# Kernel optimization log

Hardware: AMD Instinct MI355X
Metric: run time of the kernel (lower is better)

Reference implementation:

```python
import jax, jax.numpy as jnp
import numpy as np
import math

EMB = 768
B, S = 8, 2048

def setup_inputs() -> dict:
    key = jax.random.key(0)
    ks = jax.random.split(key, 6)
    q = jax.random.normal(ks[0], (B, S, EMB), dtype=jnp.float32)
    k = jax.random.normal(ks[1], (B, S, EMB), dtype=jnp.float32)
    v = jax.random.normal(ks[2], (B, S, EMB), dtype=jnp.float32)
    mask = jax.random.randint(ks[3], (B, S, S), 0, 2, dtype=jnp.int32)
    # nn.Linear(emb, emb): weight [out, in], bias [out]
    bound = 1.0 / math.sqrt(EMB)
    W = jax.random.uniform(ks[4], (EMB, EMB), minval=-bound, maxval=bound, dtype=jnp.float32)
    b = jax.random.uniform(ks[5], (EMB,), minval=-bound, maxval=bound, dtype=jnp.float32)
    return {"q": q, "k": k, "v": v, "mask": mask, "W": W, "b": b}

def reference(q, k, v, mask, W, b):
    # shared linear projection (torch Linear: x @ W^T + b)
    qp = jnp.einsum('bse,oe->bso', q, W) + b
    kp = jnp.einsum('bse,oe->bso', k, W) + b
    vp = jnp.einsum('bse,oe->bso', v, W) + b
    scores = jnp.einsum('bqe,bke->bqk', qp, kp) / math.sqrt(EMB)  # [B,S,S]
    scores = jnp.where(mask == 1, -jnp.inf, scores)
    attn = jax.nn.softmax(scores, axis=-1)
    return jnp.einsum('bqk,bke->bqe', attn, vp)
```

## Files before the change

kernel.cpp:

```cpp
#include <hip/hip_runtime.h>
#include <hip/hip_bf16.h>
#include <stdint.h>

#define B_ 8
#define S_ 2048
#define E_ 768

typedef __attribute__((ext_vector_type(4))) float f32x4;
typedef __attribute__((ext_vector_type(8))) short bf16x8;

#define A_TILE_USH (256 * 64)
#define B_TILE_USH (128 * 64)

__device__ __forceinline__ unsigned short f2bf(float f) {
  union { float f; unsigned u; } v; v.f = f;
  unsigned r = v.u + 0x7FFFu + ((v.u >> 16) & 1u);
  return (unsigned short)(r >> 16);
}

__device__ __forceinline__ void gll16(const void* g, void* l) {
  __builtin_amdgcn_global_load_lds((const __attribute__((address_space(1))) void*)g,
                                   (__attribute__((address_space(3))) void*)l, 16, 0, 0);
}

__device__ __forceinline__ void stage_tile(const char* Ab, const char* Bb,
                                           int ldAb, int ldBb, int kt,
                                           unsigned short* As, unsigned short* Bs, int tid) {
#pragma unroll
  for (int i = 0; i < 4; ++i) {
    const unsigned lin = (unsigned)i * 8192u + (unsigned)tid * 16u;
    const unsigned row = lin >> 7, cb = lin & 127u;
    const unsigned cbs = cb ^ ((row & 7u) << 4);
    gll16(Ab + (size_t)row * ldAb + (size_t)kt * 128 + cbs, (char*)As + lin);
  }
#pragma unroll
  for (int i = 0; i < 2; ++i) {
    const unsigned lin = (unsigned)i * 8192u + (unsigned)tid * 16u;
    const unsigned row = lin >> 7, cb = lin & 127u;
    const unsigned cbs = cb ^ ((row & 7u) << 4);
    gll16(Bb + (size_t)row * ldBb + (size_t)kt * 128 + cbs, (char*)Bs + lin);
  }
}

__device__ __forceinline__ void compute_tile(const unsigned short* As, const unsigned short* Bs,
                                             int wm, int wn, int lane, f32x4 (&acc)[4][4]) {
  bf16x8 af[4][2], bv[4][2];
#pragma unroll
  for (int m = 0; m < 4; ++m) {
    const int row = wm * 64 + m * 16 + (lane & 15);
#pragma unroll
    for (int ks = 0; ks < 2; ++ks) {
      const unsigned cb = ((unsigned)ks * 64u + (unsigned)(lane >> 4) * 16u) ^ (((unsigned)row & 7u) << 4);
      af[m][ks] = *reinterpret_cast<const bf16x8*>((const char*)As + row * 128 + cb);
    }
  }
#pragma unroll
  for (int n = 0; n < 4; ++n) {
    const int row = wn * 64 + n * 16 + (lane & 15);
#pragma unroll
    for (int ks = 0; ks < 2; ++ks) {
      const unsigned cb = ((unsigned)ks * 64u + (unsigned)(lane >> 4) * 16u) ^ (((unsigned)row & 7u) << 4);
      bv[n][ks] = *reinterpret_cast<const bf16x8*>((const char*)Bs + row * 128 + cb);
    }
  }
  __builtin_amdgcn_s_setprio(1);
#pragma unroll
  for (int ks = 0; ks < 2; ++ks)
#pragma unroll
    for (int m = 0; m < 4; ++m)
#pragma unroll
      for (int n = 0; n < 4; ++n)
        acc[m][n] = __builtin_amdgcn_mfma_f32_16x16x32_bf16(af[m][ks], bv[n][ks], acc[m][n], 0, 0, 0);
  __builtin_amdgcn_s_setprio(0);
}

__device__ __forceinline__ void gemm_pipe(const char* Ab, const char* Bb, int ldAb, int ldBb,
                                          int NT, unsigned short* AsAll, unsigned short* BsAll,
                                          int tid, int wm, int wn, int lane, f32x4 (&acc)[4][4]) {
  stage_tile(Ab, Bb, ldAb, ldBb, 0, AsAll, BsAll, tid);
  stage_tile(Ab, Bb, ldAb, ldBb, 1, AsAll + A_TILE_USH, BsAll + B_TILE_USH, tid);
  asm volatile("s_waitcnt vmcnt(6)" ::: "memory");
  __builtin_amdgcn_s_barrier();
  __builtin_amdgcn_sched_barrier(0);
  for (int kt = 0; kt < NT; ++kt) {
    const int bk = kt % 3;
    if (kt + 2 < NT) {
      const int bs = (kt + 2) % 3;
      stage_tile(Ab, Bb, ldAb, ldBb, kt + 2, AsAll + bs * A_TILE_USH, BsAll + bs * B_TILE_USH, tid);
    }
    compute_tile(AsAll + bk * A_TILE_USH, BsAll + bk * B_TILE_USH, wm, wn, lane, acc);
    if (kt + 1 < NT) {
      if (kt + 2 < NT) asm volatile("s_waitcnt vmcnt(6) lgkmcnt(0)" ::: "memory");
      else             asm volatile("s_waitcnt vmcnt(0) lgkmcnt(0)" ::: "memory");
      __builtin_amdgcn_s_barrier();
      __builtin_amdgcn_sched_barrier(0);
    }
  }
}

__global__ __launch_bounds__(256) void k_maskpack(const int* __restrict__ mask,
                                                  unsigned long long* __restrict__ mbits) {
  const int nwords = B_ * S_ * (S_ / 64);
  const int wave = (blockIdx.x * 256 + threadIdx.x) >> 6;
  const int lane = threadIdx.x & 63;
  const int nwaves = gridDim.x * 4;
#pragma unroll 4
  for (int w = wave; w < nwords; w += nwaves) {
    int mk = mask[(size_t)w * 64 + lane];
    unsigned long long bal = __ballot(mk == 1);
    if (lane == 0) mbits[w] = bal;
  }
}

__global__ __launch_bounds__(256) void k_proj(const float* __restrict__ qin,
                                              const float* __restrict__ kin,
                                              const float* __restrict__ vin,
                                              const float* __restrict__ W,
                                              const float* __restrict__ bias,
                                              unsigned short* __restrict__ qp,
                                              unsigned short* __restrict__ kp,
                                              unsigned short* __restrict__ vp) {
  __shared__ __attribute__((aligned(16))) unsigned short As[128 * 32];
  __shared__ __attribute__((aligned(16))) unsigned short Bs[128 * 32];
  const int tid = threadIdx.x;
  const int lane = tid & 63;
  const int wid = tid >> 6;
  const int wr = (wid >> 1) * 64;
  const int wc = (wid & 1) * 64;
  const int r0 = blockIdx.x * 128;
  const int c0 = blockIdx.y * 128;
  const int z = blockIdx.z;
  const float* X = (z == 0) ? qin : ((z == 1) ? kin : vin);
  unsigned short* O = (z == 0) ? qp : ((z == 1) ? kp : vp);

  f32x4 acc[4][4] = {};

  for (int k0 = 0; k0 < E_; k0 += 32) {
#pragma unroll
    for (int i = 0; i < 4; ++i) {
      int f = i * 256 + tid;
      int row = f >> 3, c4 = f & 7;
      float4 a = *reinterpret_cast<const float4*>(&X[(size_t)(r0 + row) * E_ + k0 + c4 * 4]);
      float4 w = *reinterpret_cast<const float4*>(&W[(size_t)(c0 + row) * E_ + k0 + c4 * 4]);
      uint2 pa, pw;
      pa.x = (unsigned)f2bf(a.x) | ((unsigned)f2bf(a.y) << 16);
      pa.y = (unsigned)f2bf(a.z) | ((unsigned)f2bf(a.w) << 16);
      pw.x = (unsigned)f2bf(w.x) | ((unsigned)f2bf(w.y) << 16);
      pw.y = (unsigned)f2bf(w.z) | ((unsigned)f2bf(w.w) << 16);
      *reinterpret_cast<uint2*>(&As[row * 32 + c4 * 4]) = pa;
      *reinterpret_cast<uint2*>(&Bs[row * 32 + c4 * 4]) = pw;
    }
    __syncthreads();
    bf16x8 af[4], bfr[4];
#pragma unroll
    for (int m = 0; m < 4; ++m)
      af[m] = *reinterpret_cast<const bf16x8*>(&As[(wr + m * 16 + (lane & 15)) * 32 + (lane >> 4) * 8]);
#pragma unroll
    for (int n = 0; n < 4; ++n)
      bfr[n] = *reinterpret_cast<const bf16x8*>(&Bs[(wc + n * 16 + (lane & 15)) * 32 + (lane >> 4) * 8]);
#pragma unroll
    for (int m = 0; m < 4; ++m)
#pragma unroll
      for (int n = 0; n < 4; ++n)
        acc[m][n] = __builtin_amdgcn_mfma_f32_16x16x32_bf16(af[m], bfr[n], acc[m][n], 0, 0, 0);
    __syncthreads();
  }

#pragma unroll
  for (int n = 0; n < 4; ++n) {
    int gc = c0 + wc + n * 16 + (lane & 15);
    float bv = bias[gc];
#pragma unroll
    for (int m = 0; m < 4; ++m) {
      int gr = r0 + wr + m * 16 + (lane >> 4) * 4;
#pragma unroll
      for (int r = 0; r < 4; ++r) {
        O[(size_t)(gr + r) * E_ + gc] = f2bf(acc[m][n][r] + bv);
      }
    }
  }
}

__global__ __launch_bounds__(256) void k_vtrans(const unsigned short* __restrict__ vp,
                                                unsigned short* __restrict__ vpT) {
  __shared__ __attribute__((aligned(16))) unsigned short t[64][72];
  const int tid = threadIdx.x;
  const int st = blockIdx.x;
  const int ot = blockIdx.y;
  const int b = blockIdx.z;
#pragma unroll
  for (int i = 0; i < 2; ++i) {
    int f = i * 256 + tid;
    int s = f >> 3, c8 = f & 7;
    uint4 vv = *reinterpret_cast<const uint4*>(
        &vp[((size_t)b * S_ + st * 64 + s) * E_ + ot * 64 + c8 * 8]);
    *reinterpret_cast<uint4*>(&t[s][c8 * 8]) = vv;
  }
  __syncthreads();
  const int o = tid >> 2;
  const int sb = (tid & 3) * 16;
  unsigned p[8];
#pragma unroll
  for (int j = 0; j < 8; ++j)
    p[j] = (unsigned)t[sb + 2 * j][o] | ((unsigned)t[sb + 2 * j + 1][o] << 16);
  uint4 w0 = make_uint4(p[0], p[1], p[2], p[3]);
  uint4 w1 = make_uint4(p[4], p[5], p[6], p[7]);
  size_t ob = ((size_t)b * E_ + ot * 64 + o) * S_ + st * 64 + sb;
  *reinterpret_cast<uint4*>(&vpT[ob]) = w0;
  *reinterpret_cast<uint4*>(&vpT[ob + 8]) = w1;
}

__global__ __launch_bounds__(512, 2) void k_scores(const unsigned short* __restrict__ qp,
                                                   const unsigned short* __restrict__ kp,
                                                   const unsigned* __restrict__ mbits,
                                                   unsigned short* __restrict__ P,
                                                   float* __restrict__ rowsum) {
  __shared__ __attribute__((aligned(16))) unsigned short AsAll[3 * A_TILE_USH];
  __shared__ __attribute__((aligned(16))) unsigned short BsAll[3 * B_TILE_USH];
  __shared__ float rlds[256][2];
  const int tid = threadIdx.x, lane = tid & 63, wid = tid >> 6;
  const int wm = wid >> 1, wn = wid & 1;
  const int qt = blockIdx.x, yt = blockIdx.y, b = blockIdx.z;
  const char* Ab = (const char*)(qp + ((size_t)b * S_ + qt * 256) * E_);
  const char* Bb = (const char*)(kp + ((size_t)b * S_ + yt * 128) * E_);
  f32x4 acc[4][4] = {};
  gemm_pipe(Ab, Bb, E_ * 2, E_ * 2, E_ / 64, AsAll, BsAll, tid, wm, wn, lane, acc);

  const float SC = (float)(1.4426950408889634 / 27.712812921102035);
  float rs[4][4];
#pragma unroll
  for (int m = 0; m < 4; ++m)
#pragma unroll
    for (int r = 0; r < 4; ++r) {
      const int grow = qt * 256 + wm * 64 + m * 16 + (lane >> 4) * 4 + r;
      const size_t rowoff = ((size_t)b * S_ + grow) * S_;
      const uint2 mb = *reinterpret_cast<const uint2*>(
          &mbits[((size_t)b * S_ + grow) * 64 + yt * 4 + wn * 2]);
      float radd = 0.f;
#pragma unroll
      for (int n = 0; n < 4; ++n) {
        const int gcol = yt * 128 + wn * 64 + n * 16 + (lane & 15);
        const unsigned wsel = (n & 2) ? mb.y : mb.x;
        const int sh = (lane & 15) + ((n & 1) << 4);
        float pv = ((wsel >> sh) & 1u) ? 0.f : __builtin_amdgcn_exp2f(acc[m][n][r] * SC);
        radd += pv;
        P[rowoff + gcol] = f2bf(pv);
      }
      rs[m][r] = radd;
    }

#pragma unroll
  for (int m = 0; m < 4; ++m)
#pragma unroll
    for (int r = 0; r < 4; ++r) {
      float vsum = rs[m][r];
      vsum += __shfl_xor(vsum, 1);
      vsum += __shfl_xor(vsum, 2);
      vsum += __shfl_xor(vsum, 4);
      vsum += __shfl_xor(vsum, 8);
      if ((lane & 15) == 0) rlds[wm * 64 + m * 16 + (lane >> 4) * 4 + r][wn] = vsum;
    }
  __syncthreads();
  if (tid < 256) {
    rowsum[(size_t)yt * (B_ * S_) + (size_t)b * S_ + qt * 256 + tid] =
        rlds[tid][0] + rlds[tid][1];
  }
}

__global__ __launch_bounds__(256) void k_invrs(const float* __restrict__ rowsum,
                                               float* __restrict__ inv_rs) {
  int i = blockIdx.x * 256 + threadIdx.x;
  float t = 0.f;
#pragma unroll
  for (int g = 0; g < 16; ++g) t += rowsum[(size_t)g * (B_ * S_) + i];
  inv_rs[i] = 1.0f / t;
}

__global__ __launch_bounds__(512, 2) void k_pv(const unsigned short* __restrict__ P,
                                               const unsigned short* __restrict__ vpT,
                                               const float* __restrict__ inv_rs,
                                               float* __restrict__ out) {
  __shared__ __attribute__((aligned(16))) unsigned short AsAll[3 * A_TILE_USH];
  __shared__ __attribute__((aligned(16))) unsigned short BsAll[3 * B_TILE_USH];
  const int tid = threadIdx.x, lane = tid & 63, wid = tid >> 6;
  const int wm = wid >> 1, wn = wid & 1;
  const int mt = blockIdx.x, yt = blockIdx.y, b = blockIdx.z;
  const char* Ab = (const char*)(P + ((size_t)b * S_ + mt * 256) * S_);
  const char* Bb = (const char*)(vpT + ((size_t)b * E_ + yt * 128) * S_);
  f32x4 acc[4][4] = {};
  gemm_pipe(Ab, Bb, S_ * 2, S_ * 2, S_ / 64, AsAll, BsAll, tid, wm, wn, lane, acc);

#pragma unroll
  for (int m = 0; m < 4; ++m)
#pragma unroll
    for (int r = 0; r < 4; ++r) {
      const int grow = mt * 256 + wm * 64 + m * 16 + (lane >> 4) * 4 + r;
      const float inv = inv_rs[b * S_ + grow];
#pragma unroll
      for (int n = 0; n < 4; ++n) {
        const int gcol = yt * 128 + wn * 64 + n * 16 + (lane & 15);
        out[((size_t)b * S_ + grow) * E_ + gcol] = acc[m][n][r] * inv;
      }
    }
}

extern "C" void kernel_launch(void* const* d_in, const int* in_sizes, int n_in,
                              void* d_out, int out_size, void* d_ws, size_t ws_size,
                              hipStream_t stream) {
  const float* q = (const float*)d_in[0];
  const float* k = (const float*)d_in[1];
  const float* v = (const float*)d_in[2];
  const int* mask = (const int*)d_in[3];
  const float* W = (const float*)d_in[4];
  const float* bias = (const float*)d_in[5];
  float* out = (float*)d_out;
  char* ws = (char*)d_ws;

  unsigned short* qp = (unsigned short*)(ws + 0);
  unsigned short* kp = (unsigned short*)(ws + 25165824);
  unsigned short* vpT = (unsigned short*)(ws + 50331648);
  unsigned short* P = (unsigned short*)(ws + 75497472);
  unsigned short* vp_tmp = P;
  float* rowsum = (float*)(ws + 142606336);
  float* inv_rs = (float*)(ws + 143654912);
  unsigned long long* mbits = (unsigned long long*)(ws + 143720448);
  (void)in_sizes; (void)n_in; (void)out_size; (void)ws_size;

  dim3 blk(256, 1, 1);
  dim3 blk2(512, 1, 1);
  k_maskpack<<<dim3(2048, 1, 1), blk, 0, stream>>>(mask, mbits);
  k_proj<<<dim3(128, 6, 3), blk, 0, stream>>>(q, k, v, W, bias, qp, kp, vp_tmp);
  k_vtrans<<<dim3(32, 12, 8), blk, 0, stream>>>(vp_tmp, vpT);
  k_scores<<<dim3(8, 16, 8), blk2, 0, stream>>>(qp, kp, (const unsigned*)mbits, P, rowsum);
  k_invrs<<<dim3(64, 1, 1), blk, 0, stream>>>(rowsum, inv_rs);
  k_pv<<<dim3(8, 6, 8), blk2, 0, stream>>>(P, vpT, inv_rs, out);
}
```

Measured before the change: 354.7 us.

## Pipeline projection GEMM, drop mask-pack kernel, split PV tiles finer

The projection kernel now uses 512-thread blocks with a 256x128 tile, a 64-wide K step and register-staged double buffering into swizzled LDS, converting to bf16 with the packed hardware convert instruction. The separate mask bit-packing kernel is removed, and the scores epilogue reads the int mask directly. The PV GEMM uses 64-column B tiles, giving twice as many blocks to improve occupancy and wave balance. The trade-offs are reading the full int mask inside the scores epilogue, and more redundant A-tile loads in PV.

```diff
diff --git a/kernel.cpp b/kernel.cpp
--- a/kernel.cpp
+++ b/kernel.cpp
@@ -10,12 +10,11 @@
 typedef __attribute__((ext_vector_type(8))) short bf16x8;
 
 #define A_TILE_USH (256 * 64)
-#define B_TILE_USH (128 * 64)
-
-__device__ __forceinline__ unsigned short f2bf(float f) {
-  union { float f; unsigned u; } v; v.f = f;
-  unsigned r = v.u + 0x7FFFu + ((v.u >> 16) & 1u);
-  return (unsigned short)(r >> 16);
+
+__device__ __forceinline__ unsigned pk2bf(float x, float y) {
+  unsigned r;
+  asm("v_cvt_pk_bf16_f32 %0, %1, %2" : "=v"(r) : "v"(x), "v"(y));
+  return r;
 }
 
 __device__ __forceinline__ void gll16(const void* g, void* l) {
@@ -23,6 +22,7 @@
                                    (__attribute__((address_space(3))) void*)l, 16, 0, 0);
 }
 
+template <int BROWS>
 __device__ __forceinline__ void stage_tile(const char* Ab, const char* Bb,
                                            int ldAb, int ldBb, int kt,
                                            unsigned short* As, unsigned short* Bs, int tid) {
@@ -34,7 +34,7 @@
     gll16(Ab + (size_t)row * ldAb + (size_t)kt * 128 + cbs, (char*)As + lin);
   }
 #pragma unroll
-  for (int i = 0; i < 2; ++i) {
+  for (int i = 0; i < BROWS / 64; ++i) {
     const unsigned lin = (unsigned)i * 8192u + (unsigned)tid * 16u;
     const unsigned row = lin >> 7, cb = lin & 127u;
     const unsigned cbs = cb ^ ((row & 7u) << 4);
@@ -42,9 +42,10 @@
   }
 }
 
+template <int NACC>
 __device__ __forceinline__ void compute_tile(const unsigned short* As, const unsigned short* Bs,
-                                             int wm, int wn, int lane, f32x4 (&acc)[4][4]) {
-  bf16x8 af[4][2], bv[4][2];
+                                             int wm, int wn, int lane, f32x4 (&acc)[4][NACC]) {
+  bf16x8 af[4][2], bv[NACC][2];
 #pragma unroll
   for (int m = 0; m < 4; ++m) {
     const int row = wm * 64 + m * 16 + (lane & 15);
@@ -55,8 +56,8 @@
     }
   }
 #pragma unroll
-  for (int n = 0; n < 4; ++n) {
-    const int row = wn * 64 + n * 16 + (lane & 15);
+  for (int n = 0; n < NACC; ++n) {
+    const int row = wn * (NACC * 16) + n * 16 + (lane & 15);
 #pragma unroll
     for (int ks = 0; ks < 2; ++ks) {
       const unsigned cb = ((unsigned)ks * 64u + (unsigned)(lane >> 4) * 16u) ^ (((unsigned)row & 7u) << 4);
@@ -69,116 +70,161 @@
 #pragma unroll
     for (int m = 0; m < 4; ++m)
 #pragma unroll
-      for (int n = 0; n < 4; ++n)
+      for (int n = 0; n < NACC; ++n)
         acc[m][n] = __builtin_amdgcn_mfma_f32_16x16x32_bf16(af[m][ks], bv[n][ks], acc[m][n], 0, 0, 0);
   __builtin_amdgcn_s_setprio(0);
 }
 
+template <int BROWS, int NACC>
 __device__ __forceinline__ void gemm_pipe(const char* Ab, const char* Bb, int ldAb, int ldBb,
                                           int NT, unsigned short* AsAll, unsigned short* BsAll,
-                                          int tid, int wm, int wn, int lane, f32x4 (&acc)[4][4]) {
-  stage_tile(Ab, Bb, ldAb, ldBb, 0, AsAll, BsAll, tid);
-  stage_tile(Ab, Bb, ldAb, ldBb, 1, AsAll + A_TILE_USH, BsAll + B_TILE_USH, tid);
-  asm volatile("s_waitcnt vmcnt(6)" ::: "memory");
+                                          int tid, int wm, int wn, int lane,
+                                          f32x4 (&acc)[4][NACC]) {
+  constexpr int BT = BROWS * 64;
+  constexpr int L = 4 + BROWS / 64;
+  stage_tile<BROWS>(Ab, Bb, ldAb, ldBb, 0, AsAll, BsAll, tid);
+  stage_tile<BROWS>(Ab, Bb, ldAb, ldBb, 1, AsAll + A_TILE_USH, BsAll + BT, tid);
+  if constexpr (L == 6) asm volatile("s_waitcnt vmcnt(6)" ::: "memory");
+  else                  asm volatile("s_waitcnt vmcnt(5)" ::: "memory");
   __builtin_amdgcn_s_barrier();
   __builtin_amdgcn_sched_barrier(0);
   for (int kt = 0; kt < NT; ++kt) {
     const int bk = kt % 3;
     if (kt + 2 < NT) {
       const int bs = (kt + 2) % 3;
-      stage_tile(Ab, Bb, ldAb, ldBb, kt + 2, AsAll + bs * A_TILE_USH, BsAll + bs * B_TILE_USH, tid);
-    }
-    compute_tile(AsAll + bk * A_TILE_USH, BsAll + bk * B_TILE_USH, wm, wn, lane, acc);
+      stage_tile<BROWS>(Ab, Bb, ldAb, ldBb, kt + 2, AsAll + bs * A_TILE_USH, BsAll + bs * BT, tid);
+    }
+    compute_tile<NACC>(AsAll + bk * A_TILE_USH, BsAll + bk * BT, wm, wn, lane, acc);
     if (kt + 1 < NT) {
-      if (kt + 2 < NT) asm volatile("s_waitcnt vmcnt(6) lgkmcnt(0)" ::: "memory");
-      else             asm volatile("s_waitcnt vmcnt(0) lgkmcnt(0)" ::: "memory");
+      if (kt + 2 < NT) {
+        if constexpr (L == 6) asm volatile("s_waitcnt vmcnt(6) lgkmcnt(0)" ::: "memory");
+        else                  asm volatile("s_waitcnt vmcnt(5) lgkmcnt(0)" ::: "memory");
+      } else {
+        asm volatile("s_waitcnt vmcnt(0) lgkmcnt(0)" ::: "memory");
+      }
       __builtin_amdgcn_s_barrier();
       __builtin_amdgcn_sched_barrier(0);
     }
   }
 }
 
-__global__ __launch_bounds__(256) void k_maskpack(const int* __restrict__ mask,
-                                                  unsigned long long* __restrict__ mbits) {
-  const int nwords = B_ * S_ * (S_ / 64);
-  const int wave = (blockIdx.x * 256 + threadIdx.x) >> 6;
-  const int lane = threadIdx.x & 63;
-  const int nwaves = gridDim.x * 4;
-#pragma unroll 4
-  for (int w = wave; w < nwords; w += nwaves) {
-    int mk = mask[(size_t)w * 64 + lane];
-    unsigned long long bal = __ballot(mk == 1);
-    if (lane == 0) mbits[w] = bal;
-  }
-}
-
-__global__ __launch_bounds__(256) void k_proj(const float* __restrict__ qin,
-                                              const float* __restrict__ kin,
-                                              const float* __restrict__ vin,
-                                              const float* __restrict__ W,
-                                              const float* __restrict__ bias,
-                                              unsigned short* __restrict__ qp,
-                                              unsigned short* __restrict__ kp,
-                                              unsigned short* __restrict__ vp) {
-  __shared__ __attribute__((aligned(16))) unsigned short As[128 * 32];
-  __shared__ __attribute__((aligned(16))) unsigned short Bs[128 * 32];
-  const int tid = threadIdx.x;
-  const int lane = tid & 63;
-  const int wid = tid >> 6;
-  const int wr = (wid >> 1) * 64;
-  const int wc = (wid & 1) * 64;
-  const int r0 = blockIdx.x * 128;
+__global__ __launch_bounds__(512, 2) void k_proj(const float* __restrict__ qin,
+                                                 const float* __restrict__ kin,
+                                                 const float* __restrict__ vin,
+                                                 const float* __restrict__ W,
+                                                 const float* __restrict__ bias,
+                                                 unsigned short* __restrict__ qp,
+                                                 unsigned short* __restrict__ kp,
+                                                 unsigned short* __restrict__ vp) {
+  __shared__ __attribute__((aligned(16))) unsigned short As[2][256 * 64];
+  __shared__ __attribute__((aligned(16))) unsigned short Bs[2][128 * 64];
+  const int tid = threadIdx.x, lane = tid & 63, wid = tid >> 6;
+  const int wm = wid >> 1, wn = wid & 1;
+  const int bx = blockIdx.x;
+  const int z = bx >> 6;
+  const int r0 = (bx & 63) * 256;
   const int c0 = blockIdx.y * 128;
-  const int z = blockIdx.z;
   const float* X = (z == 0) ? qin : ((z == 1) ? kin : vin);
   unsigned short* O = (z == 0) ? qp : ((z == 1) ? kp : vp);
 
   f32x4 acc[4][4] = {};
-
-  for (int k0 = 0; k0 < E_; k0 += 32) {
-#pragma unroll
-    for (int i = 0; i < 4; ++i) {
-      int f = i * 256 + tid;
-      int row = f >> 3, c4 = f & 7;
-      float4 a = *reinterpret_cast<const float4*>(&X[(size_t)(r0 + row) * E_ + k0 + c4 * 4]);
-      float4 w = *reinterpret_cast<const float4*>(&W[(size_t)(c0 + row) * E_ + k0 + c4 * 4]);
-      uint2 pa, pw;
-      pa.x = (unsigned)f2bf(a.x) | ((unsigned)f2bf(a.y) << 16);
-      pa.y = (unsigned)f2bf(a.z) | ((unsigned)f2bf(a.w) << 16);
-      pw.x = (unsigned)f2bf(w.x) | ((unsigned)f2bf(w.y) << 16);
-      pw.y = (unsigned)f2bf(w.z) | ((unsigned)f2bf(w.w) << 16);
-      *reinterpret_cast<uint2*>(&As[row * 32 + c4 * 4]) = pa;
-      *reinterpret_cast<uint2*>(&Bs[row * 32 + c4 * 4]) = pw;
-    }
-    __syncthreads();
-    bf16x8 af[4], bfr[4];
-#pragma unroll
-    for (int m = 0; m < 4; ++m)
-      af[m] = *reinterpret_cast<const bf16x8*>(&As[(wr + m * 16 + (lane & 15)) * 32 + (lane >> 4) * 8]);
-#pragma unroll
-    for (int n = 0; n < 4; ++n)
-      bfr[n] = *reinterpret_cast<const bf16x8*>(&Bs[(wc + n * 16 + (lane & 15)) * 32 + (lane >> 4) * 8]);
-#pragma unroll
-    for (int m = 0; m < 4; ++m)
-#pragma unroll
-      for (int n = 0; n < 4; ++n)
-        acc[m][n] = __builtin_amdgcn_mfma_f32_16x16x32_bf16(af[m], bfr[n], acc[m][n], 0, 0, 0);
-    __syncthreads();
-  }
-
-#pragma unroll
-  for (int n = 0; n < 4; ++n) {
-    int gc = c0 + wc + n * 16 + (lane & 15);
-    float bv = bias[gc];
-#pragma unroll
-    for (int m = 0; m < 4; ++m) {
-      int gr = r0 + wr + m * 16 + (lane >> 4) * 4;
-#pragma unroll
-      for (int r = 0; r < 4; ++r) {
-        O[(size_t)(gr + r) * E_ + gc] = f2bf(acc[m][n][r] + bv);
-      }
-    }
-  }
+  float4 ra[8], rb[4];
+  const int NT = E_ / 64;
+
+#pragma unroll
+  for (int i = 0; i < 8; ++i) {
+    int idx = i * 512 + tid;
+    ra[i] = *reinterpret_cast<const float4*>(&X[(size_t)(r0 + (idx >> 4)) * E_ + (idx & 15) * 4]);
+  }
+#pragma unroll
+  for (int i = 0; i < 4; ++i) {
+    int idx = i * 512 + tid;
+    rb[i] = *reinterpret_cast<const float4*>(&W[(size_t)(c0 + (idx >> 4)) * E_ + (idx & 15) * 4]);
+  }
+  asm volatile("s_waitcnt vmcnt(0)" ::: "memory");
+#pragma unroll
+  for (int i = 0; i < 8; ++i) {
+    int idx = i * 512 + tid, row = idx >> 4, c4 = idx & 15;
+    uint2 p;
+    p.x = pk2bf(ra[i].x, ra[i].y);
+    p.y = pk2bf(ra[i].z, ra[i].w);
+    unsigned off = ((unsigned)(row * 128 + c4 * 8)) ^ (((unsigned)row & 7u) << 4);
+    *reinterpret_cast<uint2*>((char*)As[0] + off) = p;
+  }
+#pragma unroll
+  for (int i = 0; i < 4; ++i) {
+    int idx = i * 512 + tid, row = idx >> 4, c4 = idx & 15;
+    uint2 p;
+    p.x = pk2bf(rb[i].x, rb[i].y);
+    p.y = pk2bf(rb[i].z, rb[i].w);
+    unsigned off = ((unsigned)(row * 128 + c4 * 8)) ^ (((unsigned)row & 7u) << 4);
+    *reinterpret_cast<uint2*>((char*)Bs[0] + off) = p;
+  }
+  asm volatile("s_waitcnt lgkmcnt(0)" ::: "memory");
+  __builtin_amdgcn_s_barrier();
+  __builtin_amdgcn_sched_barrier(0);
+
+  for (int kt = 0; kt < NT; ++kt) {
+    if (kt + 1 < NT) {
+      const int kc = (kt + 1) * 64;
+#pragma unroll
+      for (int i = 0; i < 8; ++i) {
+        int idx = i * 512 + tid;
+        ra[i] = *reinterpret_cast<const float4*>(
+            &X[(size_t)(r0 + (idx >> 4)) * E_ + kc + (idx & 15) * 4]);
+      }
+#pragma unroll
+      for (int i = 0; i < 4; ++i) {
+        int idx = i * 512 + tid;
+        rb[i] = *reinterpret_cast<const float4*>(
+            &W[(size_t)(c0 + (idx >> 4)) * E_ + kc + (idx & 15) * 4]);
+      }
+    }
+    __builtin_amdgcn_sched_barrier(0);
+    compute_tile<4>(As[kt & 1], Bs[kt & 1], wm, wn, lane, acc);
+    if (kt + 1 < NT) {
+      const int nb = (kt + 1) & 1;
+      asm volatile("s_waitcnt vmcnt(0)" ::: "memory");
+#pragma unroll
+      for (int i = 0; i < 8; ++i) {
+        int idx = i * 512 + tid, row = idx >> 4, c4 = idx & 15;
+        uint2 p;
+        p.x = pk2bf(ra[i].x, ra[i].y);
+        p.y = pk2bf(ra[i].z, ra[i].w);
+        unsigned off = ((unsigned)(row * 128 + c4 * 8)) ^ (((unsigned)row & 7u) << 4);
+        *reinterpret_cast<uint2*>((char*)As[nb] + off) = p;
+      }
+#pragma unroll
+      for (int i = 0; i < 4; ++i) {
+        int idx = i * 512 + tid, row = idx >> 4, c4 = idx & 15;
+        uint2 p;
+        p.x = pk2bf(rb[i].x, rb[i].y);
+        p.y = pk2bf(rb[i].z, rb[i].w);
+        unsigned off = ((unsigned)(row * 128 + c4 * 8)) ^ (((unsigned)row & 7u) << 4);
+        *reinterpret_cast<uint2*>((char*)Bs[nb] + off) = p;
+      }
+      asm volatile("s_waitcnt lgkmcnt(0)" ::: "memory");
+      __builtin_amdgcn_s_barrier();
+      __builtin_amdgcn_sched_barrier(0);
+    }
+  }
+
+  float bcol[4];
+#pragma unroll
+  for (int n = 0; n < 4; ++n) bcol[n] = bias[c0 + wn * 64 + n * 16 + (lane & 15)];
+#pragma unroll
+  for (int m = 0; m < 4; ++m)
+#pragma unroll
+    for (int r = 0; r < 4; ++r) {
+      const int row = r0 + wm * 64 + m * 16 + (lane >> 4) * 4 + r;
+      const int colb = c0 + wn * 64 + (lane & 15);
+      unsigned pkA = pk2bf(acc[m][0][r] + bcol[0], acc[m][1][r] + bcol[1]);
+      unsigned pkB = pk2bf(acc[m][2][r] + bcol[2], acc[m][3][r] + bcol[3]);
+      O[(size_t)row * E_ + colb]      = (unsigned short)pkA;
+      O[(size_t)row * E_ + colb + 16] = (unsigned short)(pkA >> 16);
+      O[(size_t)row * E_ + colb + 32] = (unsigned short)pkB;
+      O[(size_t)row * E_ + colb + 48] = (unsigned short)(pkB >> 16);
+    }
 }
 
 __global__ __launch_bounds__(256) void k_vtrans(const unsigned short* __restrict__ vp,
@@ -212,11 +258,11 @@
 
 __global__ __launch_bounds__(512, 2) void k_scores(const unsigned short* __restrict__ qp,
                                                    const unsigned short* __restrict__ kp,
-                                                   const unsigned* __restrict__ mbits,
+                                                   const int* __restrict__ mask,
                                                    unsigned short* __restrict__ P,
                                                    float* __restrict__ rowsum) {
   __shared__ __attribute__((aligned(16))) unsigned short AsAll[3 * A_TILE_USH];
-  __shared__ __attribute__((aligned(16))) unsigned short BsAll[3 * B_TILE_USH];
+  __shared__ __attribute__((aligned(16))) unsigned short BsAll[3 * 128 * 64];
   __shared__ float rlds[256][2];
   const int tid = threadIdx.x, lane = tid & 63, wid = tid >> 6;
   const int wm = wid >> 1, wn = wid & 1;
@@ -224,7 +270,7 @@
   const char* Ab = (const char*)(qp + ((size_t)b * S_ + qt * 256) * E_);
   const char* Bb = (const char*)(kp + ((size_t)b * S_ + yt * 128) * E_);
   f32x4 acc[4][4] = {};
-  gemm_pipe(Ab, Bb, E_ * 2, E_ * 2, E_ / 64, AsAll, BsAll, tid, wm, wn, lane, acc);
+  gemm_pipe<128, 4>(Ab, Bb, E_ * 2, E_ * 2, E_ / 64, AsAll, BsAll, tid, wm, wn, lane, acc);
 
   const float SC = (float)(1.4426950408889634 / 27.712812921102035);
   float rs[4][4];
@@ -234,19 +280,22 @@
     for (int r = 0; r < 4; ++r) {
       const int grow = qt * 256 + wm * 64 + m * 16 + (lane >> 4) * 4 + r;
       const size_t rowoff = ((size_t)b * S_ + grow) * S_;
-      const uint2 mb = *reinterpret_cast<const uint2*>(
-          &mbits[((size_t)b * S_ + grow) * 64 + yt * 4 + wn * 2]);
-      float radd = 0.f;
-#pragma unroll
-      for (int n = 0; n < 4; ++n) {
-        const int gcol = yt * 128 + wn * 64 + n * 16 + (lane & 15);
-        const unsigned wsel = (n & 2) ? mb.y : mb.x;
-        const int sh = (lane & 15) + ((n & 1) << 4);
-        float pv = ((wsel >> sh) & 1u) ? 0.f : __builtin_amdgcn_exp2f(acc[m][n][r] * SC);
-        radd += pv;
-        P[rowoff + gcol] = f2bf(pv);
-      }
-      rs[m][r] = radd;
+      const int cbase = yt * 128 + wn * 64 + (lane & 15);
+      const int mk0 = mask[rowoff + cbase];
+      const int mk1 = mask[rowoff + cbase + 16];
+      const int mk2 = mask[rowoff + cbase + 32];
+      const int mk3 = mask[rowoff + cbase + 48];
+      float p0 = (mk0 == 1) ? 0.f : __builtin_amdgcn_exp2f(acc[m][0][r] * SC);
+      float p1 = (mk1 == 1) ? 0.f : __builtin_amdgcn_exp2f(acc[m][1][r] * SC);
+      float p2 = (mk2 == 1) ? 0.f : __builtin_amdgcn_exp2f(acc[m][2][r] * SC);
+      float p3 = (mk3 == 1) ? 0.f : __builtin_amdgcn_exp2f(acc[m][3][r] * SC);
+      unsigned pkA = pk2bf(p0, p1);
+      unsigned pkB = pk2bf(p2, p3);
+      P[rowoff + cbase]      = (unsigned short)pkA;
+      P[rowoff + cbase + 16] = (unsigned short)(pkA >> 16);
+      P[rowoff + cbase + 32] = (unsigned short)pkB;
+      P[rowoff + cbase + 48] = (unsigned short)(pkB >> 16);
+      rs[m][r] = (p0 + p1) + (p2 + p3);
     }
 
 #pragma unroll
@@ -281,14 +330,14 @@
                                                const float* __restrict__ inv_rs,
                                                float* __restrict__ out) {
   __shared__ __attribute__((aligned(16))) unsigned short AsAll[3 * A_TILE_USH];
-  __shared__ __attribute__((aligned(16))) unsigned short BsAll[3 * B_TILE_USH];
+  __shared__ __attribute__((aligned(16))) unsigned short BsAll[3 * 64 * 64];
   const int tid = threadIdx.x, lane = tid & 63, wid = tid >> 6;
   const int wm = wid >> 1, wn = wid & 1;
   const int mt = blockIdx.x, yt = blockIdx.y, b = blockIdx.z;
   const char* Ab = (const char*)(P + ((size_t)b * S_ + mt * 256) * S_);
-  const char* Bb = (const char*)(vpT + ((size_t)b * E_ + yt * 128) * S_);
-  f32x4 acc[4][4] = {};
-  gemm_pipe(Ab, Bb, S_ * 2, S_ * 2, S_ / 64, AsAll, BsAll, tid, wm, wn, lane, acc);
+  const char* Bb = (const char*)(vpT + ((size_t)b * E_ + yt * 64) * S_);
+  f32x4 acc[4][2] = {};
+  gemm_pipe<64, 2>(Ab, Bb, S_ * 2, S_ * 2, S_ / 64, AsAll, BsAll, tid, wm, wn, lane, acc);
 
 #pragma unroll
   for (int m = 0; m < 4; ++m)
@@ -296,11 +345,9 @@
     for (int r = 0; r < 4; ++r) {
       const int grow = mt * 256 + wm * 64 + m * 16 + (lane >> 4) * 4 + r;
       const float inv = inv_rs[b * S_ + grow];
-#pragma unroll
-      for (int n = 0; n < 4; ++n) {
-        const int gcol = yt * 128 + wn * 64 + n * 16 + (lane & 15);
-        out[((size_t)b * S_ + grow) * E_ + gcol] = acc[m][n][r] * inv;
-      }
+      const int gcol = yt * 64 + wn * 32 + (lane & 15);
+      out[((size_t)b * S_ + grow) * E_ + gcol]      = acc[m][0][r] * inv;
+      out[((size_t)b * S_ + grow) * E_ + gcol + 16] = acc[m][1][r] * inv;
     }
 }
 
@@ -323,15 +370,13 @@
   unsigned short* vp_tmp = P;
   float* rowsum = (float*)(ws + 142606336);
   float* inv_rs = (float*)(ws + 143654912);
-  unsigned long long* mbits = (unsigned long long*)(ws + 143720448);
   (void)in_sizes; (void)n_in; (void)out_size; (void)ws_size;
 
   dim3 blk(256, 1, 1);
   dim3 blk2(512, 1, 1);
-  k_maskpack<<<dim3(2048, 1, 1), blk, 0, stream>>>(mask, mbits);
-  k_proj<<<dim3(128, 6, 3), blk, 0, stream>>>(q, k, v, W, bias, qp, kp, vp_tmp);
+  k_proj<<<dim3(192, 6, 1), blk2, 0, stream>>>(q, k, v, W, bias, qp, kp, vp_tmp);
   k_vtrans<<<dim3(32, 12, 8), blk, 0, stream>>>(vp_tmp, vpT);
-  k_scores<<<dim3(8, 16, 8), blk2, 0, stream>>>(qp, kp, (const unsigned*)mbits, P, rowsum);
+  k_scores<<<dim3(8, 16, 8), blk2, 0, stream>>>(qp, kp, mask, P, rowsum);
   k_invrs<<<dim3(64, 1, 1), blk, 0, stream>>>(rowsum, inv_rs);
-  k_pv<<<dim3(8, 6, 8), blk2, 0, stream>>>(P, vpT, inv_rs, out);
-}
+  k_pv<<<dim3(8, 12, 8), blk2, 0, stream>>>(P, vpT, inv_rs, out);
+}
```

Result: slower. 387.7 us (+9.3%).
